# Kernel optimization log

Measured on AMD Instinct MI355X. Metric: run time of the kernel, lower is better.

## Reference

```python
import jax, jax.numpy as jnp
import numpy as np

SL, BS, HS = 2048, 2, 1024
FFN, E, TOP_K = 4096, 8, 2


def setup_inputs() -> dict:
    key = jax.random.key(0)
    k1, k2, k3, k4, k5 = jax.random.split(key, 5)
    x = jax.random.normal(k1, (SL, BS, HS), dtype=jnp.float32)
    expert_weights = jax.random.uniform(k2, (SL * BS, TOP_K), dtype=jnp.float32)
    expert_indices = jax.random.randint(k3, (SL * BS, TOP_K), 0, E, dtype=jnp.int32)
    w1 = jax.random.normal(k4, (E, HS, FFN), dtype=jnp.float32) * 0.02
    w2 = jax.random.normal(k5, (E, FFN, HS), dtype=jnp.float32) * 0.02
    return {"x": x, "expert_weights": expert_weights,
            "expert_indices": expert_indices, "w1": w1, "w2": w2}


def reference(x, expert_weights, expert_indices, w1, w2):
    # Dropless MoE: y[t] = sum_k expert_weights[t,k] * MLP_{expert_indices[t,k]}(x[t])
    # Equivalent to megablocks sort/gather/grouped-GEMM/scatter pipeline, expressed
    # as a fixed loop over the (small) expert axis with masked weighted combine.
    sl, bs, hs = x.shape
    xf = x.reshape(-1, hs)                       # [T, hs]
    ew = expert_weights.reshape(xf.shape[0], -1)  # [T, k]
    ei = expert_indices.reshape(xf.shape[0], -1)  # [T, k]
    out = jnp.zeros_like(xf)
    for e in range(w1.shape[0]):
        h = jnp.dot(jax.nn.gelu(jnp.dot(xf, w1[e])), w2[e])   # [T, hs]
        coef = jnp.sum(jnp.where(ei == e, ew, 0.0), axis=-1)  # [T]
        out = out + coef[:, None] * h
    return out.reshape(sl, bs, hs)
```

## Files before the change

kernel.cpp:

```cpp
#include <hip/hip_runtime.h>
#include <stdint.h>

#define SLEN 2048
#define BSZ  2
#define HSZ  1024
#define FFND 4096
#define NEXP 8
#define TOPK 2
#define NTOK (SLEN*BSZ)
#define NSLOT (NTOK*TOPK)

#define BM 128
#define BN 128
#define BK 32

using short8 = __attribute__((ext_vector_type(8))) short;
using f32x4  = __attribute__((ext_vector_type(4))) float;

typedef __attribute__((address_space(1))) const unsigned int gu32;
typedef __attribute__((address_space(3))) unsigned int lu32;

__device__ inline void async_copy16(const void* g, void* l){
  __builtin_amdgcn_global_load_lds((gu32*)g, (lu32*)l, 16, 0, 0);
}

__device__ inline unsigned short f2bf(float f){
  unsigned u = __builtin_bit_cast(unsigned, f);
  u += 0x7FFFu + ((u >> 16) & 1u);
  return (unsigned short)(u >> 16);
}

__device__ inline float gelu_tanh(float x){
  float u = 0.7978845608028654f * (x + 0.044715f * x * x * x);
  return 0.5f * x * (1.0f + tanhf(u));
}


__global__ void k_count(const int* __restrict__ ei, int* __restrict__ counts){
  int i = blockIdx.x * blockDim.x + threadIdx.x;
  if (i < NSLOT) atomicAdd(&counts[ei[i]], 1);
}

__global__ void k_scan(const int* __restrict__ counts, int* __restrict__ offsets,
                       int* __restrict__ fill){
  if (threadIdx.x == 0 && blockIdx.x == 0){
    int acc = 0;
    for (int e = 0; e < NEXP; e++){ offsets[e] = acc; fill[e] = acc; acc += counts[e]; }
  }
}

__global__ void k_assign(const int* __restrict__ ei, const float* __restrict__ ew,
                         int* __restrict__ fill, int* __restrict__ rowT,
                         float* __restrict__ rowC){
  int i = blockIdx.x * blockDim.x + threadIdx.x;
  if (i < NSLOT){
    int e = ei[i];
    int slot = atomicAdd(&fill[e], 1);
    rowT[slot] = i >> 1;
    rowC[slot] = ew[i];
  }
}

__global__ void k_gather(const float* __restrict__ x, const int* __restrict__ rowT,
                         unsigned short* __restrict__ Xg){
  int slot = blockIdx.x;
  int t = rowT[slot];
  int c = threadIdx.x * 4;
  float4 v = *(const float4*)(x + (size_t)t * HSZ + c);
  ushort4 o;
  o.x = f2bf(v.x); o.y = f2bf(v.y); o.z = f2bf(v.z); o.w = f2bf(v.w);
  *(ushort4*)(Xg + (size_t)slot * HSZ + c) = o;
}

__global__ __launch_bounds__(256) void k_transpose(const float* __restrict__ src,
                                                   unsigned short* __restrict__ dst,
                                                   int R, int C){
  __shared__ unsigned short tile[64][65];
  const int tid = threadIdx.x;
  src += (size_t)blockIdx.z * R * C;
  dst += (size_t)blockIdx.z * R * C;
  const int r0 = blockIdx.y * 64, c0 = blockIdx.x * 64;
  #pragma unroll
  for (int p = 0; p < 4; p++){
    int r  = p * 16 + (tid >> 4);
    int cc = (tid & 15) * 4;
    float4 v = *(const float4*)(src + (size_t)(r0 + r) * C + c0 + cc);
    tile[r][cc]   = f2bf(v.x);
    tile[r][cc+1] = f2bf(v.y);
    tile[r][cc+2] = f2bf(v.z);
    tile[r][cc+3] = f2bf(v.w);
  }
  __syncthreads();
  #pragma unroll
  for (int p = 0; p < 4; p++){
    int c  = p * 16 + (tid >> 4);
    int rr = (tid & 15) * 4;
    ushort4 o;
    o.x = tile[rr][c]; o.y = tile[rr+1][c]; o.z = tile[rr+2][c]; o.w = tile[rr+3][c];
    *(ushort4*)(dst + (size_t)(c0 + c) * R + r0 + rr) = o;
  }
}

__device__ inline void gemm_core(const unsigned short* __restrict__ Ag, int lda, int rows,
                                 const unsigned short* __restrict__ Bg, int ldb, int K,
                                 unsigned short* As, unsigned short* Bs,
                                 f32x4 acc[4][4])
{
  const int tid  = threadIdx.x;
  const int lane = tid & 63;
  const int wid  = tid >> 6;
  const int wm   = (wid & 1) * 64;
  const int wn   = (wid >> 1) * 64;
  const int q    = lane >> 4;
  const int l16  = lane & 15;

  for (int k0 = 0; k0 < K; k0 += BK){
    #pragma unroll
    for (int p = 0; p < 2; p++){
      int c  = (wid * 2 + p) * 64 + lane;
      int r  = c >> 2;
      int kp = (c & 3) * 8;
      int ra = min(r, rows - 1);
      async_copy16(Ag + (size_t)ra * lda + k0 + kp, As + (wid * 2 + p) * 512);
      async_copy16(Bg + (size_t)r  * ldb + k0 + kp, Bs + (wid * 2 + p) * 512);
    }
    __syncthreads();

    short8 af[4], bfr[4];
    #pragma unroll
    for (int i = 0; i < 4; i++)
      af[i] = *(const short8*)(As + (wm + i * 16 + l16) * BK + q * 8);
    #pragma unroll
    for (int j = 0; j < 4; j++)
      bfr[j] = *(const short8*)(Bs + (wn + j * 16 + l16) * BK + q * 8);

    #pragma unroll
    for (int i = 0; i < 4; i++)
      #pragma unroll
      for (int j = 0; j < 4; j++)
        acc[i][j] = __builtin_amdgcn_mfma_f32_16x16x32_bf16(af[i], bfr[j], acc[i][j], 0, 0, 0);
    __syncthreads();
  }
}

__global__ __launch_bounds__(256) void k_gemm1(const unsigned short* __restrict__ Xg,
                                               const unsigned short* __restrict__ Wt1,
                                               unsigned short* __restrict__ H,
                                               const int* __restrict__ counts,
                                               const int* __restrict__ offsets)
{
  __shared__ unsigned short As[BM * BK];
  __shared__ unsigned short Bs[BN * BK];
  const int e    = blockIdx.z;
  const int cnt  = counts[e];
  const int mblk = blockIdx.y;
  if (mblk * BM >= cnt) return;
  const int n0   = blockIdx.x * BN;
  const int row0 = offsets[e] + mblk * BM;
  const int rows = min(BM, cnt - mblk * BM);

  f32x4 acc[4][4] = {};
  gemm_core(Xg + (size_t)row0 * HSZ, HSZ, rows,
            Wt1 + (size_t)e * HSZ * FFND + (size_t)n0 * HSZ, HSZ, HSZ, As, Bs, acc);

  const int lane = threadIdx.x & 63, wid = threadIdx.x >> 6;
  const int wm = (wid & 1) * 64, wn = (wid >> 1) * 64;
  const int q = lane >> 4, l16 = lane & 15;
  #pragma unroll
  for (int i = 0; i < 4; i++)
    #pragma unroll
    for (int j = 0; j < 4; j++)
      #pragma unroll
      for (int r = 0; r < 4; r++){
        int row = wm + i * 16 + q * 4 + r;
        if (row < rows){
          int col = wn + j * 16 + l16;
          H[(size_t)(row0 + row) * FFND + n0 + col] = f2bf(gelu_tanh(acc[i][j][r]));
        }
      }
}

__global__ __launch_bounds__(256) void k_gemm2(const unsigned short* __restrict__ H,
                                               const unsigned short* __restrict__ Wt2,
                                               float* __restrict__ out,
                                               const int* __restrict__ counts,
                                               const int* __restrict__ offsets,
                                               const int* __restrict__ rowT,
                                               const float* __restrict__ rowC)
{
  __shared__ unsigned short As[BM * BK];
  __shared__ unsigned short Bs[BN * BK];
  const int e    = blockIdx.z;
  const int cnt  = counts[e];
  const int mblk = blockIdx.y;
  if (mblk * BM >= cnt) return;
  const int n0   = blockIdx.x * BN;
  const int row0 = offsets[e] + mblk * BM;
  const int rows = min(BM, cnt - mblk * BM);

  f32x4 acc[4][4] = {};
  gemm_core(H + (size_t)row0 * FFND, FFND, rows,
            Wt2 + (size_t)e * FFND * HSZ + (size_t)n0 * FFND, FFND, FFND, As, Bs, acc);

  const int lane = threadIdx.x & 63, wid = threadIdx.x >> 6;
  const int wm = (wid & 1) * 64, wn = (wid >> 1) * 64;
  const int q = lane >> 4, l16 = lane & 15;
  #pragma unroll
  for (int i = 0; i < 4; i++)
    #pragma unroll
    for (int j = 0; j < 4; j++)
      #pragma unroll
      for (int r = 0; r < 4; r++){
        int row = wm + i * 16 + q * 4 + r;
        if (row < rows){
          int g = row0 + row;
          int col = wn + j * 16 + l16;
          atomicAdd(out + (size_t)rowT[g] * HSZ + n0 + col, rowC[g] * acc[i][j][r]);
        }
      }
}

static inline size_t align_up(size_t v, size_t a){ return (v + a - 1) & ~(a - 1); }

extern "C" void kernel_launch(void* const* d_in, const int* in_sizes, int n_in,
                              void* d_out, int out_size, void* d_ws, size_t ws_size,
                              hipStream_t stream) {
  const float* x  = (const float*)d_in[0];
  const float* ew = (const float*)d_in[1];
  const int*   ei = (const int*)d_in[2];
  const float* w1 = (const float*)d_in[3];
  const float* w2 = (const float*)d_in[4];
  float* out = (float*)d_out;

  char* base = (char*)d_ws;
  size_t off = 0;
  int* counts  = (int*)(base + off); off += 64;
  int* fill    = (int*)(base + off); off += 64;
  int* offsets = (int*)(base + off); off = align_up(off + 64, 4096);
  int* rowT    = (int*)(base + off); off += (size_t)NSLOT * 4;
  float* rowC  = (float*)(base + off); off = align_up(off + (size_t)NSLOT * 4, 1 << 20);
  unsigned short* Xg  = (unsigned short*)(base + off); off = align_up(off + (size_t)NSLOT * HSZ * 2, 1 << 20);
  unsigned short* H   = (unsigned short*)(base + off); off = align_up(off + (size_t)NSLOT * FFND * 2, 1 << 20);
  unsigned short* Wt1 = (unsigned short*)(base + off); off = align_up(off + (size_t)NEXP * HSZ * FFND * 2, 1 << 20);
  unsigned short* Wt2 = (unsigned short*)(base + off); off += (size_t)NEXP * FFND * HSZ * 2;
  (void)ws_size;

  hipMemsetAsync(d_out, 0, (size_t)out_size * sizeof(float), stream);
  hipMemsetAsync(counts, 0, 64, stream);

  k_count <<<NSLOT / 256, 256, 0, stream>>>(ei, counts);
  k_scan  <<<1, 64, 0, stream>>>(counts, offsets, fill);
  k_assign<<<NSLOT / 256, 256, 0, stream>>>(ei, ew, fill, rowT, rowC);
  k_gather<<<NSLOT, 256, 0, stream>>>(x, rowT, Xg);

  k_transpose<<<dim3(FFND / 64, HSZ / 64, NEXP), 256, 0, stream>>>(w1, Wt1, HSZ, FFND);
  k_transpose<<<dim3(HSZ / 64, FFND / 64, NEXP), 256, 0, stream>>>(w2, Wt2, FFND, HSZ);

  k_gemm1<<<dim3(FFND / BN, 64, NEXP), 256, 0, stream>>>(Xg, Wt1, H, counts, offsets);
  k_gemm2<<<dim3(HSZ  / BN, 64, NEXP), 256, 0, stream>>>(H, Wt2, out, counts, offsets, rowT, rowC);
}
```

Before: 679.8 us.

## Split-K gemm2, stage gemm1 epilogue via LDS, merge weight transposes

The second grouped GEMM is split into two K halves so twice as many blocks run. They accumulate through the existing atomicAdd into the output, which doubles the atomic traffic. The first GEMM's epilogue now writes GELU results to a per-wave LDS scratch region and stores them to H as 16-byte vectors, replacing scattered 2-byte stores. The two weight transpose launches are merged into one kernel to save a launch.

```diff
diff --git a/kernel.cpp b/kernel.cpp
--- a/kernel.cpp
+++ b/kernel.cpp
@@ -13,6 +13,8 @@
 #define BM 128
 #define BN 128
 #define BK 32
+#define SPLITK 2
+#define KS (FFND / SPLITK)
 
 using short8 = __attribute__((ext_vector_type(8))) short;
 using f32x4  = __attribute__((ext_vector_type(4))) float;
@@ -72,14 +74,24 @@
   *(ushort4*)(Xg + (size_t)slot * HSZ + c) = o;
 }
 
-__global__ __launch_bounds__(256) void k_transpose(const float* __restrict__ src,
-                                                   unsigned short* __restrict__ dst,
-                                                   int R, int C){
+__global__ __launch_bounds__(256) void k_transpose2(const float* __restrict__ w1,
+                                                    const float* __restrict__ w2,
+                                                    unsigned short* __restrict__ Wt1,
+                                                    unsigned short* __restrict__ Wt2){
   __shared__ unsigned short tile[64][65];
   const int tid = threadIdx.x;
-  src += (size_t)blockIdx.z * R * C;
-  dst += (size_t)blockIdx.z * R * C;
-  const int r0 = blockIdx.y * 64, c0 = blockIdx.x * 64;
+  int z = blockIdx.y;
+  const float* src; unsigned short* dst; int R, C, r0, c0;
+  if (z < NEXP){
+    src = w1 + (size_t)z * HSZ * FFND; dst = Wt1 + (size_t)z * HSZ * FFND;
+    R = HSZ; C = FFND;
+    c0 = (blockIdx.x & 63) * 64; r0 = (blockIdx.x >> 6) * 64;
+  } else {
+    z -= NEXP;
+    src = w2 + (size_t)z * FFND * HSZ; dst = Wt2 + (size_t)z * FFND * HSZ;
+    R = FFND; C = HSZ;
+    c0 = (blockIdx.x & 15) * 64; r0 = (blockIdx.x >> 4) * 64;
+  }
   #pragma unroll
   for (int p = 0; p < 4; p++){
     int r  = p * 16 + (tid >> 4);
@@ -149,8 +161,9 @@
                                                const int* __restrict__ counts,
                                                const int* __restrict__ offsets)
 {
-  __shared__ unsigned short As[BM * BK];
-  __shared__ unsigned short Bs[BN * BK];
+  __shared__ unsigned short smem[BM * BK + BN * BK];
+  unsigned short* As = smem;
+  unsigned short* Bs = smem + BM * BK;
   const int e    = blockIdx.z;
   const int cnt  = counts[e];
   const int mblk = blockIdx.y;
@@ -166,18 +179,25 @@
   const int lane = threadIdx.x & 63, wid = threadIdx.x >> 6;
   const int wm = (wid & 1) * 64, wn = (wid >> 1) * 64;
   const int q = lane >> 4, l16 = lane & 15;
-  #pragma unroll
-  for (int i = 0; i < 4; i++)
+
+  unsigned short* scr = smem + wid * (16 * 68);
+  #pragma unroll
+  for (int i = 0; i < 4; i++){
     #pragma unroll
     for (int j = 0; j < 4; j++)
       #pragma unroll
-      for (int r = 0; r < 4; r++){
-        int row = wm + i * 16 + q * 4 + r;
-        if (row < rows){
-          int col = wn + j * 16 + l16;
-          H[(size_t)(row0 + row) * FFND + n0 + col] = f2bf(gelu_tanh(acc[i][j][r]));
-        }
-      }
+      for (int r = 0; r < 4; r++)
+        scr[(q * 4 + r) * 68 + j * 16 + l16] = f2bf(gelu_tanh(acc[i][j][r]));
+    #pragma unroll
+    for (int p = 0; p < 2; p++){
+      int rr = p * 8 + (lane >> 3);
+      int cc = (lane & 7) * 8;
+      short8 v = *(const short8*)(scr + rr * 68 + cc);
+      int grow = wm + i * 16 + rr;
+      if (grow < rows)
+        *(short8*)(H + (size_t)(row0 + grow) * FFND + n0 + wn + cc) = v;
+    }
+  }
 }
 
 __global__ __launch_bounds__(256) void k_gemm2(const unsigned short* __restrict__ H,
@@ -190,7 +210,8 @@
 {
   __shared__ unsigned short As[BM * BK];
   __shared__ unsigned short Bs[BN * BK];
-  const int e    = blockIdx.z;
+  const int e    = blockIdx.z >> 1;
+  const int s    = blockIdx.z & 1;
   const int cnt  = counts[e];
   const int mblk = blockIdx.y;
   if (mblk * BM >= cnt) return;
@@ -199,8 +220,9 @@
   const int rows = min(BM, cnt - mblk * BM);
 
   f32x4 acc[4][4] = {};
-  gemm_core(H + (size_t)row0 * FFND, FFND, rows,
-            Wt2 + (size_t)e * FFND * HSZ + (size_t)n0 * FFND, FFND, FFND, As, Bs, acc);
+  gemm_core(H + (size_t)row0 * FFND + (size_t)s * KS, FFND, rows,
+            Wt2 + (size_t)e * FFND * HSZ + (size_t)n0 * FFND + (size_t)s * KS,
+            FFND, KS, As, Bs, acc);
 
   const int lane = threadIdx.x & 63, wid = threadIdx.x >> 6;
   const int wm = (wid & 1) * 64, wn = (wid >> 1) * 64;
@@ -253,9 +275,8 @@
   k_assign<<<NSLOT / 256, 256, 0, stream>>>(ei, ew, fill, rowT, rowC);
   k_gather<<<NSLOT, 256, 0, stream>>>(x, rowT, Xg);
 
-  k_transpose<<<dim3(FFND / 64, HSZ / 64, NEXP), 256, 0, stream>>>(w1, Wt1, HSZ, FFND);
-  k_transpose<<<dim3(HSZ / 64, FFND / 64, NEXP), 256, 0, stream>>>(w2, Wt2, FFND, HSZ);
+  k_transpose2<<<dim3(1024, 2 * NEXP), 256, 0, stream>>>(w1, w2, Wt1, Wt2);
 
   k_gemm1<<<dim3(FFND / BN, 64, NEXP), 256, 0, stream>>>(Xg, Wt1, H, counts, offsets);
-  k_gemm2<<<dim3(HSZ  / BN, 64, NEXP), 256, 0, stream>>>(H, Wt2, out, counts, offsets, rowT, rowC);
-}
+  k_gemm2<<<dim3(HSZ / BN, 64, NEXP * SPLITK), 256, 0, stream>>>(H, Wt2, out, counts, offsets, rowT, rowC);
+}
```

Result: slower. 700.6 us (+3.1%).
